# Optimization experiments

Hardware: AMD Instinct MI355X
Metric: run time of the kernel (lower is better)

Reference implementation:

```python
import jax, jax.numpy as jnp
import numpy as np

H = 8          # num heads
LN_EPS = 1e-5  # torch LayerNorm default

_SHAPES = {
    'src': (1024, 8, 256), 'pos': (1024, 8, 256), 'query_embed': (80, 8, 256), 'cam_mask': (8, 80, 1024),
    'enc_qkv_w': (2, 768, 256), 'enc_qkv_b': (2, 768), 'enc_out_w': (2, 256, 256), 'enc_out_b': (2, 256),
    'enc_ln1_g': (2, 256), 'enc_ln1_b': (2, 256),
    'enc_ff1_w': (2, 2048, 256), 'enc_ff1_b': (2, 2048), 'enc_ff2_w': (2, 256, 2048), 'enc_ff2_b': (2, 256),
    'enc_ln2_g': (2, 256), 'enc_ln2_b': (2, 256),
    'dec_sa_qkv_w': (2, 768, 256), 'dec_sa_qkv_b': (2, 768), 'dec_sa_out_w': (2, 256, 256), 'dec_sa_out_b': (2, 256),
    'dec_ln1_g': (2, 256), 'dec_ln1_b': (2, 256),
    'dec_ca_qkv_w': (2, 768, 256), 'dec_ca_qkv_b': (2, 768), 'dec_ca_out_w': (2, 256, 256), 'dec_ca_out_b': (2, 256),
    'dec_ln2_g': (2, 256), 'dec_ln2_b': (2, 256),
    'dec_ff1_w': (2, 2048, 256), 'dec_ff1_b': (2, 2048), 'dec_ff2_w': (2, 256, 2048), 'dec_ff2_b': (2, 256),
    'dec_ln3_g': (2, 256), 'dec_ln3_b': (2, 256),
    'dec_norm_g': (256,), 'dec_norm_b': (256,),
}


def setup_inputs() -> dict:
    key = jax.random.key(0)
    out = {}
    for i, (name, sh) in enumerate(_SHAPES.items()):
        k = jax.random.fold_in(key, i)
        if name.endswith('_g'):
            out[name] = jnp.ones(sh, jnp.float32)
        elif name.endswith('ln1_b') or name.endswith('ln2_b') or name.endswith('ln3_b') or name == 'dec_norm_b':
            out[name] = jnp.zeros(sh, jnp.float32)
        else:
            scale = 1.0 if name in ('src', 'pos', 'query_embed', 'cam_mask') else 0.02
            out[name] = jax.random.normal(k, sh, dtype=jnp.float32) * scale
    return out


def layer_norm(x, g, b):
    mu = jnp.mean(x, axis=-1, keepdims=True)
    var = jnp.mean(jnp.square(x - mu), axis=-1, keepdims=True)
    return (x - mu) * jax.lax.rsqrt(var + LN_EPS) * g + b


def mha(q_in, k_in, v_in, qkv_w, qkv_b, out_w, out_b, bias=None):
    # q_in: [L,B,D], k_in/v_in: [S,B,D]; torch layout: projections are x @ W.T + b
    L, B, D = q_in.shape
    S = k_in.shape[0]
    hd = D // H
    wq, wk, wv = qkv_w[:D], qkv_w[D:2 * D], qkv_w[2 * D:]
    bq, bk, bv = qkv_b[:D], qkv_b[D:2 * D], qkv_b[2 * D:]
    q = (q_in @ wq.T + bq).reshape(L, B, H, hd).transpose(1, 2, 0, 3)  # [B,H,L,hd]
    k = (k_in @ wk.T + bk).reshape(S, B, H, hd).transpose(1, 2, 0, 3)  # [B,H,S,hd]
    v = (v_in @ wv.T + bv).reshape(S, B, H, hd).transpose(1, 2, 0, 3)
    logits = jnp.einsum('bhld,bhsd->bhls', q, k) * (1.0 / np.sqrt(hd))
    if bias is not None:
        logits = logits + bias[:, None, :, :]  # CAM bias broadcast over heads
    attn = jax.nn.softmax(logits, axis=-1)
    o = jnp.einsum('bhls,bhsd->bhld', attn, v).transpose(2, 0, 1, 3).reshape(L, B, D)
    return o @ out_w.T + out_b


def reference(src, pos, query_embed, cam_mask,
              enc_qkv_w, enc_qkv_b, enc_out_w, enc_out_b, enc_ln1_g, enc_ln1_b,
              enc_ff1_w, enc_ff1_b, enc_ff2_w, enc_ff2_b, enc_ln2_g, enc_ln2_b,
              dec_sa_qkv_w, dec_sa_qkv_b, dec_sa_out_w, dec_sa_out_b, dec_ln1_g, dec_ln1_b,
              dec_ca_qkv_w, dec_ca_qkv_b, dec_ca_out_w, dec_ca_out_b, dec_ln2_g, dec_ln2_b,
              dec_ff1_w, dec_ff1_b, dec_ff2_w, dec_ff2_b, dec_ln3_g, dec_ln3_b,
              dec_norm_g, dec_norm_b):
    n_enc = enc_qkv_w.shape[0]
    n_dec = dec_sa_qkv_w.shape[0]
    # --- encoder (post-norm DETR style, pos added to q,k) ---
    mem = src
    for i in range(n_enc):
        qk = mem + pos
        a = mha(qk, qk, mem, enc_qkv_w[i], enc_qkv_b[i], enc_out_w[i], enc_out_b[i])
        mem = layer_norm(mem + a, enc_ln1_g[i], enc_ln1_b[i])
        f = jax.nn.relu(mem @ enc_ff1_w[i].T + enc_ff1_b[i]) @ enc_ff2_w[i].T + enc_ff2_b[i]
        mem = layer_norm(mem + f, enc_ln2_g[i], enc_ln2_b[i])
    # --- decoder: tgt starts at zeros (Q2L), query_embed is query_pos ---
    tgt = jnp.zeros_like(query_embed)
    for i in range(n_dec):
        qk = tgt + query_embed
        sa = mha(qk, qk, tgt, dec_sa_qkv_w[i], dec_sa_qkv_b[i], dec_sa_out_w[i], dec_sa_out_b[i])
        tgt = layer_norm(tgt + sa, dec_ln1_g[i], dec_ln1_b[i])
        ca = mha(tgt + query_embed, mem + pos, mem,
                 dec_ca_qkv_w[i], dec_ca_qkv_b[i], dec_ca_out_w[i], dec_ca_out_b[i],
                 bias=cam_mask)  # MA: CAM-derived additive attention bias [B,L,S]
        tgt = layer_norm(tgt + ca, dec_ln2_g[i], dec_ln2_b[i])
        f = jax.nn.relu(tgt @ dec_ff1_w[i].T + dec_ff1_b[i]) @ dec_ff2_w[i].T + dec_ff2_b[i]
        tgt = layer_norm(tgt + f, dec_ln3_g[i], dec_ln3_b[i])
    out = layer_norm(tgt, dec_norm_g, dec_norm_b)
    return out[None]  # [1, L, B, D] as in TransformerDecoder's output.unsqueeze(0)
```

## Files before the change

### kernel.cpp

```cpp
#include <hip/hip_runtime.h>
#include <hip/hip_bf16.h>
#include <cstdint>
#include <cstddef>

typedef __hip_bfloat16 bf16;
typedef float f4 __attribute__((ext_vector_type(4)));
typedef float f32x4 __attribute__((ext_vector_type(4)));
typedef short s8v __attribute__((ext_vector_type(8)));
typedef unsigned short u16x4 __attribute__((ext_vector_type(4)));
typedef unsigned short u16x8 __attribute__((ext_vector_type(8)));

#define LN_EPS 1e-5f
#define LOG2E 1.4426950408889634f

#if __has_builtin(__builtin_amdgcn_exp2f)
__device__ __forceinline__ float EXP2(float x) { return __builtin_amdgcn_exp2f(x); }
#else
__device__ __forceinline__ float EXP2(float x) {
  float r; asm("v_exp_f32 %0, %1" : "=v"(r) : "v"(x)); return r;
}
#endif

__device__ __forceinline__ void async_cp16(const void* g, void* lds) {
  __builtin_amdgcn_global_load_lds(
      (const __attribute__((address_space(1))) unsigned int*)g,
      (__attribute__((address_space(3))) unsigned int*)lds, 16, 0, 0);
}

__device__ __forceinline__ uint32_t pkbf(float lo, float hi) {
#if __has_builtin(__builtin_amdgcn_perm)
  uint32_t l = __builtin_bit_cast(uint32_t, lo) + 0x8000u;
  uint32_t h = __builtin_bit_cast(uint32_t, hi) + 0x8000u;
  return __builtin_amdgcn_perm(h, l, 0x07060302u);
#else
  uint32_t l = __builtin_bit_cast(uint32_t, lo) + 0x8000u;
  uint32_t h = __builtin_bit_cast(uint32_t, hi) + 0x8000u;
  return (l >> 16) | (h & 0xFFFF0000u);
#endif
}

#define NCAST 16
struct CastArgs {
  const float* in[NCAST];
  bf16* out[NCAST];
  int end4[NCAST];
  int nseg;
};

__global__ __launch_bounds__(256) void cast_multi(CastArgs a, int total4) {
  int i = blockIdx.x * 256 + threadIdx.x;
  if (i >= total4) return;
  int s = 0;
  while (i >= a.end4[s]) ++s;
  int j = i - (s ? a.end4[s - 1] : 0);
  f4 v = ((const f4*)a.in[s])[j];
  u16x4 o;
#pragma unroll
  for (int c = 0; c < 4; ++c) {
    bf16 h = __float2bfloat16(v[c]);
    o[c] = *reinterpret_cast<unsigned short*>(&h);
  }
  ((u16x4*)a.out[s])[j] = o;
}

__global__ __launch_bounds__(256) void enc_prolog(
    const float* __restrict__ src, const float* __restrict__ pos,
    bf16* __restrict__ memb, bf16* __restrict__ qkb, int n4) {
  int i = blockIdx.x * 256 + threadIdx.x;
  if (i < n4) {
    f4 s = ((const f4*)src)[i];
    f4 p = ((const f4*)pos)[i];
    u16x4 om, oq;
#pragma unroll
    for (int j = 0; j < 4; ++j) {
      bf16 hm = __float2bfloat16(s[j]);
      bf16 hq = __float2bfloat16(s[j] + p[j]);
      om[j] = *reinterpret_cast<unsigned short*>(&hm);
      oq[j] = *reinterpret_cast<unsigned short*>(&hq);
    }
    ((u16x4*)memb)[i] = om;
    ((u16x4*)qkb)[i] = oq;
  }
}

__global__ __launch_bounds__(256) void pack_pb(const float* __restrict__ qkvb,
                                               float* __restrict__ pb) {
  int j = threadIdx.x;
  pb[j]       = qkvb[256 + j];
  pb[256 + j] = qkvb[768 + 256 + j];
  pb[512 + j] = qkvb[512 + j];
  pb[768 + j] = qkvb[768 + 512 + j];
}

__global__ __launch_bounds__(256) void sa0_row(
    const float* __restrict__ Wo, const float* __restrict__ bv,
    const float* __restrict__ bo, const float* __restrict__ g,
    const float* __restrict__ b, float* __restrict__ row_out) {
  const int j = threadIdx.x;
  float acc = bo[j];
  for (int k = 0; k < 256; k += 4) {
    f4 w = *(const f4*)(Wo + (size_t)j * 256 + k);
    f4 v = *(const f4*)(bv + k);
    acc += w[0] * v[0] + w[1] * v[1] + w[2] * v[2] + w[3] * v[3];
  }
  float s = acc, s2 = acc * acc;
#pragma unroll
  for (int off = 32; off >= 1; off >>= 1) {
    s += __shfl_down(s, off);
    s2 += __shfl_down(s2, off);
  }
  __shared__ float red[8];
  int wv = j >> 6;
  if ((j & 63) == 0) { red[wv] = s; red[4 + wv] = s2; }
  __syncthreads();
  if (j == 0) {
    float ts = red[0] + red[1] + red[2] + red[3];
    float ts2 = red[4] + red[5] + red[6] + red[7];
    float mu = ts * (1.f / 256.f);
    float var = ts2 * (1.f / 256.f) - mu * mu;
    red[0] = mu;
    red[1] = rsqrtf(var + LN_EPS);
  }
  __syncthreads();
  row_out[j] = (acc - red[0]) * red[1] * g[j] + b[j];
}

__global__ __launch_bounds__(256) void sa0_bcast(
    const float* __restrict__ row, const float* __restrict__ qe,
    float* __restrict__ tgt, bf16* __restrict__ tgtb, bf16* __restrict__ tqkb) {
  const int r = blockIdx.x, j = threadIdx.x;
  float y = row[j];
  size_t idx = (size_t)r * 256 + j;
  tgt[idx] = y;
  tgtb[idx] = __float2bfloat16(y);
  tqkb[idx] = __float2bfloat16(y + qe[idx]);
}

template <int TB, int MODE, int SPLITK>
__global__ __launch_bounds__(256, 2) void mfma_gemm(
    const bf16* __restrict__ A, const bf16* __restrict__ W,
    const float* __restrict__ bias, float* __restrict__ C,
    bf16* __restrict__ Cb, int M, int N, int K, int HL, float qscale,
    const bf16* __restrict__ A2, bf16* __restrict__ Cb2, int nyA, int secV) {
  constexpr int WM = TB / 2, WN = TB / 2;
  constexpr int MR = WM / 16, NR = WN / 16;
  constexpr int NCH = TB / 32;
  __shared__ __attribute__((aligned(16))) unsigned short SH[TB * 128];
  unsigned short (*As)[64] = (unsigned short(*)[64])SH;
  unsigned short (*Ws)[64] = (unsigned short(*)[64])(SH + TB * 64);
  const int tid = threadIdx.x;
  const int lane = tid & 63, wave = tid >> 6;
  const int wr = wave >> 1, wc = wave & 1;
  const int bm = blockIdx.x * TB, bn = blockIdx.y * TB;
  const int fr = lane & 15, fo = lane >> 4;
  const int srowi = lane >> 3;
  const int slot = lane & 7;
  const int gcol = (slot ^ srowi) * 8;

  const bf16* Aeff = (MODE == 6) ? (((int)blockIdx.y < nyA) ? A : A2) : A;

  const int kchunk = K / SPLITK;
  const int kbeg = (SPLITK > 1) ? blockIdx.z * kchunk : 0;

  f32x4 acc[MR][NR] = {};

  for (int k0 = kbeg; k0 < kbeg + kchunk; k0 += 64) {
    __syncthreads();
#pragma unroll
    for (int c = 0; c < NCH; ++c) {
      int rbase = wave * (TB / 4) + c * 8;
      int row = rbase + srowi;
      async_cp16(Aeff + (size_t)(bm + row) * K + k0 + gcol, &As[rbase][0]);
      async_cp16(W + (size_t)(bn + row) * K + k0 + gcol, &Ws[rbase][0]);
    }
    __syncthreads();
#pragma unroll
    for (int ks = 0; ks < 2; ++ks) {
      s8v a[MR], b[NR];
#pragma unroll
      for (int mi = 0; mi < MR; ++mi) {
        int row = wr * WM + mi * 16 + fr;
        a[mi] = *(const s8v*)((const char*)&As[0][0] + row * 128 +
                              ((ks * 64 + fo * 16) ^ ((row & 7) << 4)));
      }
#pragma unroll
      for (int ni = 0; ni < NR; ++ni) {
        int row = wc * WN + ni * 16 + fr;
        b[ni] = *(const s8v*)((const char*)&Ws[0][0] + row * 128 +
                              ((ks * 64 + fo * 16) ^ ((row & 7) << 4)));
      }
#pragma unroll
      for (int mi = 0; mi < MR; ++mi)
#pragma unroll
        for (int ni = 0; ni < NR; ++ni)
          acc[mi][ni] = __builtin_amdgcn_mfma_f32_16x16x32_bf16(
              a[mi], b[ni], acc[mi][ni], 0, 0, 0);
    }
  }

  const int r0 = (lane >> 4) * 4;

  if (MODE == 5 || (MODE == 6 && (bn >> 8) >= secV)) {
    __syncthreads();
    unsigned short (*T)[72] = (unsigned short(*)[72])SH;
#pragma unroll
    for (int mi = 0; mi < MR; ++mi)
#pragma unroll
      for (int ni = 0; ni < NR; ++ni) {
        int colL = wc * WN + ni * 16 + fr;
        float bv = bias[bn + colL];
#pragma unroll
        for (int r = 0; r < 4; ++r) {
          int rowL = wr * WM + mi * 16 + r0 + r;
          bf16 hv = __float2bfloat16(acc[mi][ni][r] + bv);
          T[colL][rowL] = *(unsigned short*)&hv;
        }
      }
    __syncthreads();
    bf16* Cv = (MODE == 6) ? Cb2 : Cb;
    const int secBase = (MODE == 6) ? secV : 0;
    const int lbase = bm >> 3;
#pragma unroll
    for (int jj = 0; jj < 2; ++jj) {
      int cid = tid * 2 + jj;
      int colL = cid >> 3, bb = cid & 7;
      int c = bn + colL;
      int sec = (c >> 8) - secBase, hh = (c >> 5) & 7, d = c & 31;
      u16x8 v;
#pragma unroll
      for (int l = 0; l < 8; ++l) v[l] = T[colL][bb + 8 * l];
      *(u16x8*)(Cv + (size_t)sec * ((size_t)64 * 32 * HL) +
                ((size_t)(bb * 8 + hh) * 32 + d) * HL + lbase) = v;
    }
    return;
  }

  float* Cz = (MODE == 4) ? C + (size_t)blockIdx.z * M * N : C;
#pragma unroll
  for (int mi = 0; mi < MR; ++mi) {
#pragma unroll
    for (int ni = 0; ni < NR; ++ni) {
      int col = bn + wc * WN + ni * 16 + fr;
      float bv = (MODE == 4) ? 0.f : bias[col];
#pragma unroll
      for (int r = 0; r < 4; ++r) {
        int row = bm + wr * WM + mi * 16 + r0 + r;
        float t = acc[mi][ni][r] + bv;
        if (MODE == 2) t = fmaxf(t, 0.f);
        if (MODE == 0) {
          C[(size_t)row * N + col] = t;
        } else if (MODE == 4) {
          Cz[(size_t)row * N + col] = t;
        } else if (MODE == 3 || MODE == 6) {
          int l = row >> 3, bb = row & 7;
          int sec = col >> 8, hh = (col >> 5) & 7, d = col & 31;
          if (sec == 0) t *= qscale;
          Cb[(size_t)sec * ((size_t)64 * HL * 32) +
             ((size_t)(bb * 8 + hh) * HL + l) * 32 + d] = __float2bfloat16(t);
        } else {
          Cb[(size_t)row * N + col] = __float2bfloat16(t);
        }
      }
    }
  }
}

template <int HAS_BIAS, int PARTIAL, int NW>
__global__ __launch_bounds__(NW * 64, 3) void attn_mfma(
    const bf16* __restrict__ Qh, const bf16* __restrict__ Kh,
    const bf16* __restrict__ VhT, const float* __restrict__ bias,
    bf16* __restrict__ O, float* __restrict__ PO, float* __restrict__ PM,
    float* __restrict__ PL, int L, int S, int SC) {
  __shared__ __attribute__((aligned(16))) uint32_t Ps2[NW][2][16][36];
  const int tid = threadIdx.x;
  const int lane = tid & 63, wave = tid >> 6;
  const int fr = lane & 15, fo = lane >> 4;
  const int bh = blockIdx.x;
  const int b = bh >> 3, h = bh & 7;
  const int q0 = blockIdx.y * (NW * 16) + wave * 16;
  const int q = q0 + fr;

  const int cz = PARTIAL ? blockIdx.z : 0;
  const int sb = PARTIAL ? cz * SC : 0;
  const int se = PARTIAL ? min(S, sb + SC) : S;
  const int ng = (se - sb + 63) >> 6;

  s8v qf = {};
  if (q < L) qf = *(const s8v*)(Qh + ((size_t)bh * L + q) * 32 + fo * 8);

  const float* brow = nullptr;
  if (HAS_BIAS) brow = bias + ((size_t)b * L + (q < L ? q : L - 1)) * S;

  const bf16* Kbase = Kh + (size_t)bh * S * 32;
  const bf16* Vbase = VhT + (size_t)bh * 32 * S;

  float mA = -1e30f, lsA = 0.f, mB = -1e30f, lsB = 0.f;
  f32x4 oA[2] = {}, oB[2] = {};

  for (int g = 0; g < ng; g += 2) {
    const int sA = sb + g * 64, sB = sA + 64;

    s8v kA[4], kB[4], vA[2][2], vB[2][2];
#pragma unroll
    for (int kb = 0; kb < 4; ++kb) {
      kA[kb] = *(const s8v*)(Kbase + (size_t)(sA + kb * 16 + fr) * 32 + fo * 8);
      kB[kb] = *(const s8v*)(Kbase + (size_t)(sB + kb * 16 + fr) * 32 + fo * 8);
    }
#pragma unroll
    for (int dh = 0; dh < 2; ++dh)
#pragma unroll
      for (int ks = 0; ks < 2; ++ks) {
        vA[dh][ks] = *(const s8v*)(Vbase + (size_t)(dh * 16 + fr) * S +
                                   sA + ks * 32 + fo * 8);
        vB[dh][ks] = *(const s8v*)(Vbase + (size_t)(dh * 16 + fr) * S +
                                   sB + ks * 32 + fo * 8);
      }
    f4 bA[4], bB[4];
    if (HAS_BIAS) {
#pragma unroll
      for (int kb = 0; kb < 4; ++kb) {
        bA[kb] = *(const f4*)(brow + sA + kb * 16 + 4 * fo);
        bB[kb] = *(const f4*)(brow + sB + kb * 16 + 4 * fo);
      }
    }

    float lgA[16], lgB[16];
    __builtin_amdgcn_s_setprio(1);
#pragma unroll
    for (int kb = 0; kb < 4; ++kb) {
      f32x4 z = {};
      f32x4 sa = __builtin_amdgcn_mfma_f32_16x16x32_bf16(kA[kb], qf, z, 0, 0, 0);
#pragma unroll
      for (int r = 0; r < 4; ++r) lgA[kb * 4 + r] = sa[r];
    }
#pragma unroll
    for (int kb = 0; kb < 4; ++kb) {
      f32x4 z = {};
      f32x4 sa = __builtin_amdgcn_mfma_f32_16x16x32_bf16(kB[kb], qf, z, 0, 0, 0);
#pragma unroll
      for (int r = 0; r < 4; ++r) lgB[kb * 4 + r] = sa[r];
    }
    __builtin_amdgcn_s_setprio(0);
    if (HAS_BIAS) {
#pragma unroll
      for (int i = 0; i < 16; ++i) {
        lgA[i] = fmaf(bA[i >> 2][i & 3], LOG2E, lgA[i]);
        lgB[i] = fmaf(bB[i >> 2][i & 3], LOG2E, lgB[i]);
      }
    }
    if (sB + 64 > se) {
#pragma unroll
      for (int i = 0; i < 16; ++i) {
        int keyA = sA + (i >> 2) * 16 + 4 * fo + (i & 3);
        int keyB = sB + (i >> 2) * 16 + 4 * fo + (i & 3);
        if (keyA >= se) lgA[i] = -1e30f;
        if (keyB >= se) lgB[i] = -1e30f;
      }
    }

    float tA, tB;
    {
      float a0 = fmaxf(fmaxf(lgA[0], lgA[1]), fmaxf(lgA[2], lgA[3]));
      float a1 = fmaxf(fmaxf(lgA[4], lgA[5]), fmaxf(lgA[6], lgA[7]));
      float a2 = fmaxf(fmaxf(lgA[8], lgA[9]), fmaxf(lgA[10], lgA[11]));
      float a3 = fmaxf(fmaxf(lgA[12], lgA[13]), fmaxf(lgA[14], lgA[15]));
      tA = fmaxf(fmaxf(a0, a1), fmaxf(a2, a3));
      float b0 = fmaxf(fmaxf(lgB[0], lgB[1]), fmaxf(lgB[2], lgB[3]));
      float b1 = fmaxf(fmaxf(lgB[4], lgB[5]), fmaxf(lgB[6], lgB[7]));
      float b2 = fmaxf(fmaxf(lgB[8], lgB[9]), fmaxf(lgB[10], lgB[11]));
      float b3 = fmaxf(fmaxf(lgB[12], lgB[13]), fmaxf(lgB[14], lgB[15]));
      tB = fmaxf(fmaxf(b0, b1), fmaxf(b2, b3));
    }
    tA = fmaxf(tA, __shfl_xor(tA, 16));
    tB = fmaxf(tB, __shfl_xor(tB, 16));
    tA = fmaxf(tA, __shfl_xor(tA, 32));
    tB = fmaxf(tB, __shfl_xor(tB, 32));

    float nmA = fmaxf(mA, tA), nmB = fmaxf(mB, tB);
    float rsA = EXP2(mA - nmA), rsB = EXP2(mB - nmB);
    mA = nmA; mB = nmB;

    float psA = 0.f, psB = 0.f;
#pragma unroll
    for (int i = 0; i < 16; ++i) {
      lgA[i] = EXP2(lgA[i] - nmA); psA += lgA[i];
      lgB[i] = EXP2(lgB[i] - nmB); psB += lgB[i];
    }
    lsA = lsA * rsA + psA;
    lsB = lsB * rsB + psB;

#pragma unroll
    for (int kb = 0; kb < 4; ++kb) {
      uint32_t a0 = pkbf(lgA[kb * 4 + 0], lgA[kb * 4 + 1]);
      uint32_t a1 = pkbf(lgA[kb * 4 + 2], lgA[kb * 4 + 3]);
      *(uint64_t*)&Ps2[wave][0][fr][kb * 8 + 2 * fo] =
          (uint64_t)a0 | ((uint64_t)a1 << 32);
      uint32_t b0 = pkbf(lgB[kb * 4 + 0], lgB[kb * 4 + 1]);
      uint32_t b1 = pkbf(lgB[kb * 4 + 2], lgB[kb * 4 + 3]);
      *(uint64_t*)&Ps2[wave][1][fr][kb * 8 + 2 * fo] =
          (uint64_t)b0 | ((uint64_t)b1 << 32);
    }

#pragma unroll
    for (int r = 0; r < 4; ++r) {
      oA[0][r] *= rsA; oA[1][r] *= rsA;
      oB[0][r] *= rsB; oB[1][r] *= rsB;
    }
    s8v pA[2], pB[2];
#pragma unroll
    for (int ks = 0; ks < 2; ++ks) {
      pA[ks] = *(const s8v*)&Ps2[wave][0][fr][ks * 16 + 4 * fo];
      pB[ks] = *(const s8v*)&Ps2[wave][1][fr][ks * 16 + 4 * fo];
    }
    __builtin_amdgcn_s_setprio(1);
#pragma unroll
    for (int dh = 0; dh < 2; ++dh)
#pragma unroll
      for (int ks = 0; ks < 2; ++ks) {
        oA[dh] = __builtin_amdgcn_mfma_f32_16x16x32_bf16(vA[dh][ks], pA[ks], oA[dh], 0, 0, 0);
        oB[dh] = __builtin_amdgcn_mfma_f32_16x16x32_bf16(vB[dh][ks], pB[ks], oB[dh], 0, 0, 0);
      }
    __builtin_amdgcn_s_setprio(0);
  }

  float m = fmaxf(mA, mB);
  float wA = EXP2(mA - m), wB = EXP2(mB - m);
  float lsum = lsA * wA + lsB * wB;
  f32x4 oacc[2];
#pragma unroll
  for (int dh = 0; dh < 2; ++dh)
#pragma unroll
    for (int r = 0; r < 4; ++r)
      oacc[dh][r] = oA[dh][r] * wA + oB[dh][r] * wB;

  lsum += __shfl_xor(lsum, 16);
  lsum += __shfl_xor(lsum, 32);

  if (q < L) {
    if (PARTIAL) {
      size_t pi = ((size_t)cz * 64 + bh) * L + q;
      float* po = PO + pi * 32;
#pragma unroll
      for (int dh = 0; dh < 2; ++dh) {
        f4 t2;
#pragma unroll
        for (int r = 0; r < 4; ++r) t2[r] = oacc[dh][r];
        *(f4*)(po + dh * 16 + 4 * fo) = t2;
      }
      if (fo == 0) { PM[pi] = m; PL[pi] = lsum; }
    } else {
      float inv = 1.f / lsum;
      bf16* op = O + ((size_t)q * 8 + b) * 256 + h * 32;
#pragma unroll
      for (int dh = 0; dh < 2; ++dh) {
        uint32_t w0 = pkbf(oacc[dh][0] * inv, oacc[dh][1] * inv);
        uint32_t w1 = pkbf(oacc[dh][2] * inv, oacc[dh][3] * inv);
        *(uint32_t*)(op + dh * 16 + 4 * fo) = w0;
        *(uint32_t*)(op + dh * 16 + 4 * fo + 2) = w1;
      }
    }
  }
}

__global__ __launch_bounds__(256) void attn_combine(
    const float* __restrict__ PO, const float* __restrict__ PM,
    const float* __restrict__ PL, bf16* __restrict__ O, int L, int NC) {
  int gid = blockIdx.x * 256 + threadIdx.x;
  if (gid >= 64 * L * 32) return;
  int d = gid & 31;
  int rem = gid >> 5;
  int q = rem % L, bh = rem / L;
  int b = bh >> 3, h = bh & 7;
  float M = -1e30f;
  for (int c = 0; c < NC; ++c) M = fmaxf(M, PM[((size_t)c * 64 + bh) * L + q]);
  float lsum = 0.f, o = 0.f;
  for (int c = 0; c < NC; ++c) {
    size_t pi = ((size_t)c * 64 + bh) * L + q;
    float w = EXP2(PM[pi] - M);
    lsum += PL[pi] * w;
    o += PO[pi * 32 + d] * w;
  }
  O[((size_t)q * 8 + b) * 256 + h * 32 + d] = __float2bfloat16(o / lsum);
}

__global__ __launch_bounds__(256) void ln_kernel(
    const float* __restrict__ x, const float* __restrict__ res,
    const float* __restrict__ parts, int nparts, int pstride,
    const float* __restrict__ gbias,
    const float* __restrict__ g, const float* __restrict__ b,
    float* __restrict__ out, bf16* __restrict__ outb,
    const float* __restrict__ aux, bf16* __restrict__ auxb) {
  const int row = blockIdx.x, tid = threadIdx.x;
  size_t idx = (size_t)row * 256 + tid;
  float v = x[idx];
  if (res) v += res[idx];
  if (parts) {
    for (int z = 0; z < nparts; ++z) v += parts[(size_t)z * pstride + idx];
  }
  if (gbias) v += gbias[tid];
  float s = v, s2 = v * v;
#pragma unroll
  for (int off = 32; off >= 1; off >>= 1) {
    s += __shfl_down(s, off);
    s2 += __shfl_down(s2, off);
  }
  __shared__ float red[8];
  int wv = tid >> 6;
  if ((tid & 63) == 0) { red[wv] = s; red[4 + wv] = s2; }
  __syncthreads();
  if (tid == 0) {
    float ts = red[0] + red[1] + red[2] + red[3];
    float ts2 = red[4] + red[5] + red[6] + red[7];
    float mu = ts * (1.f / 256.f);
    float var = ts2 * (1.f / 256.f) - mu * mu;
    red[0] = mu;
    red[1] = rsqrtf(var + LN_EPS);
  }
  __syncthreads();
  float y = (v - red[0]) * red[1] * g[tid] + b[tid];
  if (out) out[idx] = y;
  if (outb) outb[idx] = __float2bfloat16(y);
  if (auxb) auxb[idx] = __float2bfloat16(y + aux[idx]);
}

extern "C" void kernel_launch(void* const* d_in, const int* in_sizes, int n_in,
                              void* d_out, int out_size, void* d_ws, size_t ws_size,
                              hipStream_t stream) {
  const float* src         = (const float*)d_in[0];
  const float* pos         = (const float*)d_in[1];
  const float* query_embed = (const float*)d_in[2];
  const float* cam_mask    = (const float*)d_in[3];
  const float* enc_qkv_w   = (const float*)d_in[4];
  const float* enc_qkv_b   = (const float*)d_in[5];
  const float* enc_out_w   = (const float*)d_in[6];
  const float* enc_out_b   = (const float*)d_in[7];
  const float* enc_ln1_g   = (const float*)d_in[8];
  const float* enc_ln1_b   = (const float*)d_in[9];
  const float* enc_ff1_w   = (const float*)d_in[10];
  const float* enc_ff1_b   = (const float*)d_in[11];
  const float* enc_ff2_w   = (const float*)d_in[12];
  const float* enc_ff2_b   = (const float*)d_in[13];
  const float* enc_ln2_g   = (const float*)d_in[14];
  const float* enc_ln2_b   = (const float*)d_in[15];
  const float* dec_sa_qkv_w= (const float*)d_in[16];
  const float* dec_sa_qkv_b= (const float*)d_in[17];
  const float* dec_sa_out_w= (const float*)d_in[18];
  const float* dec_sa_out_b= (const float*)d_in[19];
  const float* dec_ln1_g   = (const float*)d_in[20];
  const float* dec_ln1_b   = (const float*)d_in[21];
  const float* dec_ca_qkv_w= (const float*)d_in[22];
  const float* dec_ca_qkv_b= (const float*)d_in[23];
  const float* dec_ca_out_w= (const float*)d_in[24];
  const float* dec_ca_out_b= (const float*)d_in[25];
  const float* dec_ln2_g   = (const float*)d_in[26];
  const float* dec_ln2_b   = (const float*)d_in[27];
  const float* dec_ff1_w   = (const float*)d_in[28];
  const float* dec_ff1_b   = (const float*)d_in[29];
  const float* dec_ff2_w   = (const float*)d_in[30];
  const float* dec_ff2_b   = (const float*)d_in[31];
  const float* dec_ln3_g   = (const float*)d_in[32];
  const float* dec_ln3_b   = (const float*)d_in[33];
  const float* dec_norm_g  = (const float*)d_in[34];
  const float* dec_norm_b  = (const float*)d_in[35];

  size_t off = 0;
  char* base = (char*)d_ws;
  auto af = [&](size_t n) { float* p = (float*)(base + off); off += n * 4; return p; };
  auto ab = [&](size_t n) { bf16*  p = (bf16*)(base + off);  off += n * 2; return p; };

  float* mem  = af(2097152);
  float* PO   = af(8388608);
  float* pm   = af(262144);
  float* pl   = af(262144);
  float* pb   = af(1024);
  float* row0 = af(256);
  float* tgt  = af(163840);
  bf16* memb  = ab(2097152);
  bf16* qkb   = ab(2097152);
  bf16* aob   = ab(2097152);
  bf16* ffb   = ab(16777216);
  bf16* bufQ  = ab(4194304);
  bf16* bufK  = ab(4194304);
  bf16* bufV  = ab(4194304);
  bf16* bufVsa= ab(172032);
  bf16* tgtb  = ab(163840);
  bf16* tqkb  = ab(163840);
  bf16* taob  = ab(163840);
  bf16* qeb   = ab(163840);
  bf16* tffb  = ab(1310720);
  bf16* w_enc_qkv = ab(393216);
  bf16* w_enc_out = ab(131072);
  bf16* w_enc_ff1 = ab(1048576);
  bf16* w_enc_ff2 = ab(1048576);
  bf16* w_sa_qkv  = ab(393216);
  bf16* w_sa_out  = ab(131072);
  bf16* w_ca_q    = ab(131072);
  bf16* w_ca_kv   = ab(262144);
  bf16* w_ca_out  = ab(131072);
  bf16* w_dec_ff1 = ab(1048576);
  bf16* w_dec_ff2 = ab(1048576);

  const float qscale = 0.17677669529663687f * LOG2E;

  {
    CastArgs ca;
    const float* ins[NCAST] = {
        enc_qkv_w, enc_out_w, enc_ff1_w, enc_ff2_w,
        dec_sa_qkv_w, dec_sa_out_w,
        dec_ca_qkv_w,
        dec_ca_qkv_w + 65536,
        dec_ca_qkv_w + 131072,
        dec_ca_qkv_w + 196608,
        dec_ca_qkv_w + 262144,
        dec_ca_qkv_w + 327680,
        dec_ca_out_w, dec_ff1_w, dec_ff2_w, query_embed};
    bf16* outs[NCAST] = {
        w_enc_qkv, w_enc_out, w_enc_ff1, w_enc_ff2,
        w_sa_qkv, w_sa_out,
        w_ca_q,
        w_ca_kv,
        w_ca_kv + 131072,
        w_ca_q + 65536,
        w_ca_kv + 65536,
        w_ca_kv + 196608,
        w_ca_out, w_dec_ff1, w_dec_ff2, qeb};
    int n4s[NCAST] = {98304, 32768, 262144, 262144, 98304, 32768,
                      16384, 16384, 16384, 16384, 16384, 16384,
                      32768, 262144, 262144, 40960};
    int acc = 0;
    for (int s = 0; s < NCAST; ++s) {
      ca.in[s] = ins[s]; ca.out[s] = outs[s];
      acc += n4s[s]; ca.end4[s] = acc;
    }
    ca.nseg = NCAST;
    cast_multi<<<(acc + 255) / 256, 256, 0, stream>>>(ca, acc);
  }
  enc_prolog<<<2048, 256, 0, stream>>>(src, pos, memb, qkb, 524288);
  pack_pb<<<1, 256, 0, stream>>>(dec_ca_qkv_b, pb);

  auto g64_head = [&](const bf16* A, const bf16* W, const float* bias, bf16* Cb,
                      int M, int N, int K, int HL, float qs) {
    mfma_gemm<64, 3, 1><<<dim3(M / 64, N / 64), 256, 0, stream>>>(
        A, W, bias, nullptr, Cb, M, N, K, HL, qs, nullptr, nullptr, 0, 0);
  };
  auto g64_relu = [&](const bf16* A, const bf16* W, const float* bias, bf16* Cb,
                      int M, int N, int K) {
    mfma_gemm<64, 2, 1><<<dim3(M / 64, N / 64), 256, 0, stream>>>(
        A, W, bias, nullptr, Cb, M, N, K, 0, 1.f, nullptr, nullptr, 0, 0);
  };
  auto g128_relu = [&](const bf16* A, const bf16* W, const float* bias, bf16* Cb,
                       int M, int N, int K) {
    mfma_gemm<128, 2, 1><<<dim3(M / 128, N / 128), 256, 0, stream>>>(
        A, W, bias, nullptr, Cb, M, N, K, 0, 1.f, nullptr, nullptr, 0, 0);
  };

  for (int i = 0; i < 2; ++i) {
    const bf16* wq = w_enc_qkv + (size_t)i * 196608;
    const float* qkvb = enc_qkv_b + (size_t)i * 768;
    mfma_gemm<64, 6, 1><<<dim3(128, 12), 256, 0, stream>>>(
        qkb, wq, qkvb, nullptr, bufQ, 8192, 768, 256, 1024, qscale,
        memb, bufV, 8, 2);
    attn_mfma<0, 0, 4><<<dim3(64, 16), 256, 0, stream>>>(
        bufQ, bufQ + 2097152, bufV, nullptr, aob, nullptr, nullptr, nullptr,
        1024, 1024, 0);
    mfma_gemm<64, 4, 2><<<dim3(128, 4, 2), 256, 0, stream>>>(
        aob, w_enc_out + (size_t)i * 65536, nullptr, PO, nullptr,
        8192, 256, 256, 0, 1.f, nullptr, nullptr, 0, 0);
    ln_kernel<<<8192, 256, 0, stream>>>((i == 0) ? src : mem, nullptr, PO, 2, 2097152,
                                        enc_out_b + i * 256,
                                        enc_ln1_g + i * 256, enc_ln1_b + i * 256,
                                        mem, memb, nullptr, nullptr);
    g128_relu(memb, w_enc_ff1 + (size_t)i * 524288, enc_ff1_b + i * 2048, ffb,
              8192, 2048, 256);
    mfma_gemm<64, 4, 2><<<dim3(128, 4, 2), 256, 0, stream>>>(
        ffb, w_enc_ff2 + (size_t)i * 524288, nullptr, PO, nullptr,
        8192, 256, 2048, 0, 1.f, nullptr, nullptr, 0, 0);
    ln_kernel<<<8192, 256, 0, stream>>>(mem, nullptr, PO, 2, 2097152,
                                        enc_ff2_b + i * 256,
                                        enc_ln2_g + i * 256, enc_ln2_b + i * 256,
                                        mem, memb, pos, qkb);
  }

  mfma_gemm<64, 6, 1><<<dim3(128, 16), 256, 0, stream>>>(
      qkb, w_ca_kv, pb, nullptr, bufK, 8192, 1024, 256, 1024, 1.f,
      memb, bufV, 8, 2);

  for (int i = 0; i < 2; ++i) {
    const float* sab = dec_sa_qkv_b + (size_t)i * 768;
    const float* cab = dec_ca_qkv_b + (size_t)i * 768;

    if (i == 0) {
      sa0_row<<<1, 256, 0, stream>>>(dec_sa_out_w, dec_sa_qkv_b + 512,
                                     dec_sa_out_b, dec_ln1_g, dec_ln1_b, row0);
      sa0_bcast<<<640, 256, 0, stream>>>(row0, query_embed, tgt, tgtb, tqkb);
    } else {
      const bf16* wsa = w_sa_qkv + (size_t)i * 196608;
      mfma_gemm<64, 6, 1><<<dim3(10, 12), 256, 0, stream>>>(
          tqkb, wsa, sab, nullptr, bufQ, 640, 768, 256, 80, qscale,
          tgtb, bufVsa, 8, 2);
      attn_mfma<0, 0, 1><<<dim3(64, 5), 64, 0, stream>>>(
          bufQ, bufQ + 163840, bufVsa, nullptr, taob, nullptr, nullptr, nullptr,
          80, 80, 0);
      mfma_gemm<64, 4, 4><<<dim3(10, 4, 4), 256, 0, stream>>>(
          taob, w_sa_out + (size_t)i * 65536, nullptr, PO, nullptr,
          640, 256, 256, 0, 1.f, nullptr, nullptr, 0, 0);
      ln_kernel<<<640, 256, 0, stream>>>(tgt, nullptr, PO, 4, 163840,
                                         dec_sa_out_b + i * 256,
                                         dec_ln1_g + i * 256, dec_ln1_b + i * 256,
                                         tgt, tgtb, query_embed, tqkb);
    }
    g64_head(tqkb, w_ca_q + (size_t)i * 65536, cab, bufQ, 640, 256, 256, 80, qscale);
    attn_mfma<1, 1, 1><<<dim3(64, 5, 4), 64, 0, stream>>>(
        bufQ, bufK + (size_t)i * 2097152, bufV + (size_t)i * 2097152, cam_mask,
        nullptr, PO + 4194304, pm, pl, 80, 1024, 256);
    attn_combine<<<640, 256, 0, stream>>>(PO + 4194304, pm, pl, taob, 80, 4);
    mfma_gemm<64, 4, 4><<<dim3(10, 4, 4), 256, 0, stream>>>(
        taob, w_ca_out + (size_t)i * 65536, nullptr, PO, nullptr,
        640, 256, 256, 0, 1.f, nullptr, nullptr, 0, 0);
    ln_kernel<<<640, 256, 0, stream>>>(tgt, nullptr, PO, 4, 163840,
                                       dec_ca_out_b + i * 256,
                                       dec_ln2_g + i * 256, dec_ln2_b + i * 256,
                                       tgt, tgtb, nullptr, nullptr);
    g64_relu(tgtb, w_dec_ff1 + (size_t)i * 524288, dec_ff1_b + i * 2048, tffb,
             640, 2048, 256);
    mfma_gemm<64, 4, 4><<<dim3(10, 4, 4), 256, 0, stream>>>(
        tffb, w_dec_ff2 + (size_t)i * 524288, nullptr, PO, nullptr,
        640, 256, 2048, 0, 1.f, nullptr, nullptr, 0, 0);
    ln_kernel<<<640, 256, 0, stream>>>(tgt, nullptr, PO, 4, 163840,
                                       dec_ff2_b + i * 256,
                                       dec_ln3_g + i * 256, dec_ln3_b + i * 256,
                                       tgt, tgtb, query_embed, tqkb);
  }

  ln_kernel<<<640, 256, 0, stream>>>(tgt, nullptr, nullptr, 0, 0, nullptr,
                                     dec_norm_g, dec_norm_b,
                                     (float*)d_out, nullptr, nullptr, nullptr);
}
```

Measured before the change: 377.1 us.

## Fuse output/FF2 projection GEMMs with residual LayerNorm in full-row tiles

Adds a gemm_ln kernel that computes a 64-row by full 256-column tile per block, so bias, residual add and LayerNorm run in the GEMM epilogue. This replaces the split-K GEMM, which wrote partial sums to a buffer, plus the separate ln_kernel pass. It removes a launch and the partial-sum traffic at each post-attention and post-FFN step. The cost is parallelism: the encoder now launches only 128 blocks and the decoder only 10, with no split-K and no double buffering. That leaves many CUs idle and risks slower GEMMs, especially the K=2048 FF2.

```diff
diff --git a/kernel.cpp b/kernel.cpp
--- a/kernel.cpp
+++ b/kernel.cpp
@@ -134,6 +134,95 @@
   tgt[idx] = y;
   tgtb[idx] = __float2bfloat16(y);
   tqkb[idx] = __float2bfloat16(y + qe[idx]);
+}
+
+__global__ __launch_bounds__(256) void gemm_ln(
+    const bf16* __restrict__ A, const bf16* __restrict__ W,
+    const float* __restrict__ bias, const float* __restrict__ res,
+    const float* __restrict__ g, const float* __restrict__ b,
+    float* __restrict__ out, bf16* __restrict__ outb,
+    const float* __restrict__ aux, bf16* __restrict__ auxb,
+    int M, int K) {
+  __shared__ __attribute__((aligned(16))) unsigned short SH[320 * 64];
+  const int tid = threadIdx.x;
+  const int lane = tid & 63, wave = tid >> 6;
+  const int fr = lane & 15, fo = lane >> 4;
+  const int srowi = lane >> 3;
+  const int slot = lane & 7;
+  const int gcol = (slot ^ srowi) * 8;
+  const int bm = blockIdx.x * 64;
+
+  f32x4 acc[16] = {};
+
+  for (int k0 = 0; k0 < K; k0 += 64) {
+    __syncthreads();
+#pragma unroll
+    for (int c = 0; c < 10; ++c) {
+      int rbase = c * 32 + wave * 8;
+      int row = rbase + srowi;
+      const bf16* src = (row < 64)
+          ? A + (size_t)(bm + row) * K + k0 + gcol
+          : W + (size_t)(row - 64) * K + k0 + gcol;
+      async_cp16(src, SH + (size_t)rbase * 64);
+    }
+    __syncthreads();
+#pragma unroll
+    for (int ks = 0; ks < 2; ++ks) {
+      int ar = wave * 16 + fr;
+      s8v a = *(const s8v*)((const char*)SH + ar * 128 +
+                            ((ks * 64 + fo * 16) ^ ((ar & 7) << 4)));
+#pragma unroll
+      for (int ni = 0; ni < 16; ++ni) {
+        int wrow = 64 + ni * 16 + fr;
+        s8v bf = *(const s8v*)((const char*)SH + wrow * 128 +
+                               ((ks * 64 + fo * 16) ^ ((wrow & 7) << 4)));
+        acc[ni] = __builtin_amdgcn_mfma_f32_16x16x32_bf16(a, bf, acc[ni], 0, 0, 0);
+      }
+    }
+  }
+
+  const int r0 = fo * 4;
+  float vv[4][16];
+#pragma unroll
+  for (int ni = 0; ni < 16; ++ni) {
+    int col = ni * 16 + fr;
+    float bv = bias[col];
+#pragma unroll
+    for (int r = 0; r < 4; ++r) {
+      int grow = bm + wave * 16 + r0 + r;
+      vv[r][ni] = acc[ni][r] + bv + res[(size_t)grow * 256 + col];
+    }
+  }
+  float mu[4], rstd[4];
+#pragma unroll
+  for (int r = 0; r < 4; ++r) {
+    float s = 0.f, s2 = 0.f;
+#pragma unroll
+    for (int ni = 0; ni < 16; ++ni) { s += vv[r][ni]; s2 += vv[r][ni] * vv[r][ni]; }
+#pragma unroll
+    for (int off = 1; off <= 8; off <<= 1) {
+      s += __shfl_xor(s, off);
+      s2 += __shfl_xor(s2, off);
+    }
+    float m = s * (1.f / 256.f);
+    float var = s2 * (1.f / 256.f) - m * m;
+    mu[r] = m;
+    rstd[r] = rsqrtf(var + LN_EPS);
+  }
+#pragma unroll
+  for (int ni = 0; ni < 16; ++ni) {
+    int col = ni * 16 + fr;
+    float gg = g[col], bb = b[col];
+#pragma unroll
+    for (int r = 0; r < 4; ++r) {
+      int grow = bm + wave * 16 + r0 + r;
+      size_t idx = (size_t)grow * 256 + col;
+      float y = (vv[r][ni] - mu[r]) * rstd[r] * gg + bb;
+      out[idx] = y;
+      outb[idx] = __float2bfloat16(y);
+      if (auxb) auxb[idx] = __float2bfloat16(y + aux[idx]);
+    }
+  }
 }
 
 template <int TB, int MODE, int SPLITK>
@@ -484,20 +573,12 @@
 }
 
 __global__ __launch_bounds__(256) void ln_kernel(
-    const float* __restrict__ x, const float* __restrict__ res,
-    const float* __restrict__ parts, int nparts, int pstride,
-    const float* __restrict__ gbias,
+    const float* __restrict__ x,
     const float* __restrict__ g, const float* __restrict__ b,
-    float* __restrict__ out, bf16* __restrict__ outb,
-    const float* __restrict__ aux, bf16* __restrict__ auxb) {
+    float* __restrict__ out) {
   const int row = blockIdx.x, tid = threadIdx.x;
   size_t idx = (size_t)row * 256 + tid;
   float v = x[idx];
-  if (res) v += res[idx];
-  if (parts) {
-    for (int z = 0; z < nparts; ++z) v += parts[(size_t)z * pstride + idx];
-  }
-  if (gbias) v += gbias[tid];
   float s = v, s2 = v * v;
 #pragma unroll
   for (int off = 32; off >= 1; off >>= 1) {
@@ -517,10 +598,7 @@
     red[1] = rsqrtf(var + LN_EPS);
   }
   __syncthreads();
-  float y = (v - red[0]) * red[1] * g[tid] + b[tid];
-  if (out) out[idx] = y;
-  if (outb) outb[idx] = __float2bfloat16(y);
-  if (auxb) auxb[idx] = __float2bfloat16(y + aux[idx]);
+  out[idx] = (v - red[0]) * red[1] * g[tid] + b[tid];
 }
 
 extern "C" void kernel_launch(void* const* d_in, const int* in_sizes, int n_in,
@@ -663,22 +741,16 @@
     attn_mfma<0, 0, 4><<<dim3(64, 16), 256, 0, stream>>>(
         bufQ, bufQ + 2097152, bufV, nullptr, aob, nullptr, nullptr, nullptr,
         1024, 1024, 0);
-    mfma_gemm<64, 4, 2><<<dim3(128, 4, 2), 256, 0, stream>>>(
-        aob, w_enc_out + (size_t)i * 65536, nullptr, PO, nullptr,
-        8192, 256, 256, 0, 1.f, nullptr, nullptr, 0, 0);
-    ln_kernel<<<8192, 256, 0, stream>>>((i == 0) ? src : mem, nullptr, PO, 2, 2097152,
-                                        enc_out_b + i * 256,
-                                        enc_ln1_g + i * 256, enc_ln1_b + i * 256,
-                                        mem, memb, nullptr, nullptr);
+    gemm_ln<<<128, 256, 0, stream>>>(
+        aob, w_enc_out + (size_t)i * 65536, enc_out_b + i * 256,
+        (i == 0) ? src : mem, enc_ln1_g + i * 256, enc_ln1_b + i * 256,
+        mem, memb, nullptr, nullptr, 8192, 256);
     g128_relu(memb, w_enc_ff1 + (size_t)i * 524288, enc_ff1_b + i * 2048, ffb,
               8192, 2048, 256);
-    mfma_gemm<64, 4, 2><<<dim3(128, 4, 2), 256, 0, stream>>>(
-        ffb, w_enc_ff2 + (size_t)i * 524288, nullptr, PO, nullptr,
-        8192, 256, 2048, 0, 1.f, nullptr, nullptr, 0, 0);
-    ln_kernel<<<8192, 256, 0, stream>>>(mem, nullptr, PO, 2, 2097152,
-                                        enc_ff2_b + i * 256,
-                                        enc_ln2_g + i * 256, enc_ln2_b + i * 256,
-                                        mem, memb, pos, qkb);
+    gemm_ln<<<128, 256, 0, stream>>>(
+        ffb, w_enc_ff2 + (size_t)i * 524288, enc_ff2_b + i * 256,
+        mem, enc_ln2_g + i * 256, enc_ln2_b + i * 256,
+        mem, memb, pos, qkb, 8192, 2048);
   }
 
   mfma_gemm<64, 6, 1><<<dim3(128, 16), 256, 0, stream>>>(
@@ -701,38 +773,27 @@
       attn_mfma<0, 0, 1><<<dim3(64, 5), 64, 0, stream>>>(
           bufQ, bufQ + 163840, bufVsa, nullptr, taob, nullptr, nullptr, nullptr,
           80, 80, 0);
-      mfma_gemm<64, 4, 4><<<dim3(10, 4, 4), 256, 0, stream>>>(
-          taob, w_sa_out + (size_t)i * 65536, nullptr, PO, nullptr,
-          640, 256, 256, 0, 1.f, nullptr, nullptr, 0, 0);
-      ln_kernel<<<640, 256, 0, stream>>>(tgt, nullptr, PO, 4, 163840,
-                                         dec_sa_out_b + i * 256,
-                                         dec_ln1_g + i * 256, dec_ln1_b + i * 256,
-                                         tgt, tgtb, query_embed, tqkb);
+      gemm_ln<<<10, 256, 0, stream>>>(
+          taob, w_sa_out + (size_t)i * 65536, dec_sa_out_b + i * 256,
+          tgt, dec_ln1_g + i * 256, dec_ln1_b + i * 256,
+          tgt, tgtb, query_embed, tqkb, 640, 256);
     }
     g64_head(tqkb, w_ca_q + (size_t)i * 65536, cab, bufQ, 640, 256, 256, 80, qscale);
     attn_mfma<1, 1, 1><<<dim3(64, 5, 4), 64, 0, stream>>>(
         bufQ, bufK + (size_t)i * 2097152, bufV + (size_t)i * 2097152, cam_mask,
-        nullptr, PO + 4194304, pm, pl, 80, 1024, 256);
-    attn_combine<<<640, 256, 0, stream>>>(PO + 4194304, pm, pl, taob, 80, 4);
-    mfma_gemm<64, 4, 4><<<dim3(10, 4, 4), 256, 0, stream>>>(
-        taob, w_ca_out + (size_t)i * 65536, nullptr, PO, nullptr,
-        640, 256, 256, 0, 1.f, nullptr, nullptr, 0, 0);
-    ln_kernel<<<640, 256, 0, stream>>>(tgt, nullptr, PO, 4, 163840,
-                                       dec_ca_out_b + i * 256,
-                                       dec_ln2_g + i * 256, dec_ln2_b + i * 256,
-                                       tgt, tgtb, nullptr, nullptr);
+        nullptr, PO, pm, pl, 80, 1024, 256);
+    attn_combine<<<640, 256, 0, stream>>>(PO, pm, pl, taob, 80, 4);
+    gemm_ln<<<10, 256, 0, stream>>>(
+        taob, w_ca_out + (size_t)i * 65536, dec_ca_out_b + i * 256,
+        tgt, dec_ln2_g + i * 256, dec_ln2_b + i * 256,
+        tgt, tgtb, nullptr, nullptr, 640, 256);
     g64_relu(tgtb, w_dec_ff1 + (size_t)i * 524288, dec_ff1_b + i * 2048, tffb,
              640, 2048, 256);
-    mfma_gemm<64, 4, 4><<<dim3(10, 4, 4), 256, 0, stream>>>(
-        tffb, w_dec_ff2 + (size_t)i * 524288, nullptr, PO, nullptr,
-        640, 256, 2048, 0, 1.f, nullptr, nullptr, 0, 0);
-    ln_kernel<<<640, 256, 0, stream>>>(tgt, nullptr, PO, 4, 163840,
-                                       dec_ff2_b + i * 256,
-                                       dec_ln3_g + i * 256, dec_ln3_b + i * 256,
-                                       tgt, tgtb, query_embed, tqkb);
-  }
-
-  ln_kernel<<<640, 256, 0, stream>>>(tgt, nullptr, nullptr, 0, 0, nullptr,
-                                     dec_norm_g, dec_norm_b,
-                                     (float*)d_out, nullptr, nullptr, nullptr);
-}
+    gemm_ln<<<10, 256, 0, stream>>>(
+        tffb, w_dec_ff2 + (size_t)i * 524288, dec_ff2_b + i * 256,
+        tgt, dec_ln3_g + i * 256, dec_ln3_b + i * 256,
+        tgt, tgtb, query_embed, tqkb, 640, 2048);
+  }
+
+  ln_kernel<<<640, 256, 0, stream>>>(tgt, dec_norm_g, dec_norm_b, (float*)d_out);
+}
```

Result: slower. 547.7 us (+45.2%).
